# Performance work log

Hardware: AMD Instinct MI355X
Metric: run time of the kernel (lower is better)

The kernel has to match this reference:

```python
import jax, jax.numpy as jnp
import numpy as np

B, S, DIM, H = 2, 2048, 1024, 16
HD = DIM // H  # 64


def setup_inputs() -> dict:
    key = jax.random.key(0)
    ks = jax.random.split(key, 7)
    sc = 1.0 / np.sqrt(DIM)
    gammas = jnp.asarray(1.0 - 2.0 ** (-5.0 - np.arange(H)), jnp.float32)  # RetNet per-head decay
    return {
        "q": jax.random.normal(ks[0], (B, S, DIM), jnp.float32),
        "k": jax.random.normal(ks[1], (B, S, DIM), jnp.float32),
        "v": jax.random.normal(ks[2], (B, S, DIM), jnp.float32),
        "W_in": jax.random.normal(ks[3], (DIM, DIM), jnp.float32) * sc,
        "b_in": jnp.zeros((DIM,), jnp.float32),
        "W_gate": jax.random.normal(ks[4], (DIM, DIM), jnp.float32) * sc,
        "b_gate": jnp.zeros((DIM,), jnp.float32),
        "W_out": jax.random.normal(ks[5], (DIM, DIM), jnp.float32) * sc,
        "b_out": jnp.zeros((DIM,), jnp.float32),
        "gammas": gammas,
    }


def _mamba(x, W_in, b_in, W_gate, b_gate, W_out, b_out):
    # Gated linear recurrence: h_t = a_t * h_{t-1} + u_t  (selective-scan style)
    u = x @ W_in + b_in          # [B,S,D]
    a = jax.nn.sigmoid(x @ W_gate + b_gate)  # [B,S,D] data-dependent decay gate

    def combine(c1, c2):
        a1, u1 = c1
        a2, u2 = c2
        return (a1 * a2, a2 * u1 + u2)

    _, h = jax.lax.associative_scan(combine, (a, u), axis=1)  # parallel scan over S
    return h @ W_out + b_out  # residual=False, dropout=0.0


def _retention(q, k, v, gammas):
    # Per-head decay-masked attention: out = ((Q K^T / sqrt(hd)) * D) V,
    # D[h,n,m] = gamma_h^(n-m) for n>=m else 0 (causal decay kernel).
    def split(x):
        return x.reshape(B, S, H, HD).transpose(0, 2, 1, 3)  # [B,H,S,HD]

    qh, kh, vh = split(q), split(k), split(v)
    idx = jnp.arange(S)
    diff = idx[:, None] - idx[None, :]                        # [S,S]
    expnt = jnp.maximum(diff, 0).astype(jnp.float32)
    D = jnp.where(diff >= 0, gammas[:, None, None] ** expnt, 0.0)  # [H,S,S]
    scores = jnp.einsum("bhnd,bhmd->bhnm", qh, kh) / np.sqrt(HD)
    out = jnp.einsum("bhnm,bhmd->bhnd", scores * D[None], vh)
    return out.transpose(0, 2, 1, 3).reshape(B, S, DIM)


def reference(q, k, v, W_in, b_in, W_gate, b_gate, W_out, b_out, gammas):
    q_proj = _mamba(q, W_in, b_in, W_gate, b_gate, W_out, b_out)
    return _retention(q_proj, k, v, gammas)
```

## Files before the change

### kernel.cpp

```cpp
#include <hip/hip_runtime.h>
#include <math.h>

#define B_  2
#define S_  2048
#define D_  1024
#define H_  16
#define HD_ 64
#define M_  (B_*S_)

typedef unsigned short ushort_t;
typedef unsigned int   uint_t;
typedef __attribute__((ext_vector_type(8))) short bf16x8;
typedef __attribute__((ext_vector_type(4))) float f32x4;

__device__ __forceinline__ ushort_t f2bf(float f) {
    uint_t u = __builtin_bit_cast(uint_t, f);
    u += 0x7FFFu + ((u >> 16) & 1u);
    return (ushort_t)(u >> 16);
}
__device__ __forceinline__ float bf2f(ushort_t h) {
    uint_t u = (uint_t)h << 16;
    return __builtin_bit_cast(float, u);
}
__device__ __forceinline__ uint_t pkt(float lo, float hi) {
    return __builtin_amdgcn_perm(__builtin_bit_cast(uint_t, hi),
                                 __builtin_bit_cast(uint_t, lo), 0x07060302u);
}
__device__ __forceinline__ void dma16(const ushort_t* g, ushort_t* l) {
    __builtin_amdgcn_global_load_lds(
        (const __attribute__((address_space(1))) uint_t*)g,
        (__attribute__((address_space(3))) uint_t*)l, 16, 0, 0);
}
__device__ __forceinline__ bf16x8 fragr(const ushort_t* base, int row, int chunk) {
    return *(const bf16x8*)&base[row * 64 + (((chunk ^ (row & 7)) << 3))];
}

__global__ __launch_bounds__(256)
void transp_cvt3(const float* __restrict__ W0, const float* __restrict__ W1,
                 const float* __restrict__ W2, ushort_t* __restrict__ T0,
                 ushort_t* __restrict__ T1, ushort_t* __restrict__ T2) {
    __shared__ float T[32][36];
    const float*  W  = (blockIdx.z == 0) ? W0 : (blockIdx.z == 1) ? W1 : W2;
    ushort_t*     WT = (blockIdx.z == 0) ? T0 : (blockIdx.z == 1) ? T1 : T2;
    const int kt = blockIdx.x, nt = blockIdx.y;
    const int t = threadIdx.x;
    const int rr = t >> 3, cc = (t & 7) * 4;
    float4 w4 = *(const float4*)(W + (size_t)(kt * 32 + rr) * D_ + nt * 32 + cc);
    T[rr][cc + 0] = w4.x; T[rr][cc + 1] = w4.y; T[rr][cc + 2] = w4.z; T[rr][cc + 3] = w4.w;
    __syncthreads();
    ushort_t o[4];
    #pragma unroll
    for (int j = 0; j < 4; ++j) o[j] = f2bf(T[cc + j][rr]);
    *(ushort4*)(WT + (size_t)(nt * 32 + rr) * D_ + kt * 32 + cc) =
        make_ushort4(o[0], o[1], o[2], o[3]);
}

__global__ __launch_bounds__(256)
void cvt_bf16(const float* __restrict__ X, ushort_t* __restrict__ Y) {
    const int i = (blockIdx.x * 256 + threadIdx.x) * 4;
    float4 x = *(const float4*)(X + i);
    *(ushort4*)(Y + i) = make_ushort4(f2bf(x.x), f2bf(x.y), f2bf(x.z), f2bf(x.w));
}

__global__ __launch_bounds__(256)
void kv_cvt_g(const float* __restrict__ K, const float* __restrict__ V,
              const float* __restrict__ gammas, ushort_t* __restrict__ Kb,
              ushort_t* __restrict__ VT, float* __restrict__ Gg) {
    __shared__ ushort_t Tv[64 * 72];
    __shared__ ushort_t Tk[64 * 72];
    const int mt = blockIdx.x, h = blockIdx.y, b = blockIdx.z;
    const int m0 = mt * 64;
    const int tid = threadIdx.x;
    const int r = tid >> 2, c0 = (tid & 3) * 16;
    const float lg = log2f(gammas[h]);
    const float gm = exp2f(-(float)r * lg);
    {
        const float* src = K + ((size_t)(b * S_ + m0 + r)) * D_ + h * HD_ + c0;
        ushort_t kb[16];
        #pragma unroll
        for (int j4 = 0; j4 < 4; ++j4) {
            float4 x = *(const float4*)(src + j4 * 4);
            kb[j4 * 4 + 0] = f2bf(x.x); kb[j4 * 4 + 1] = f2bf(x.y);
            kb[j4 * 4 + 2] = f2bf(x.z); kb[j4 * 4 + 3] = f2bf(x.w);
        }
        ushort_t* dst = Kb + ((size_t)(b * S_ + m0 + r)) * D_ + h * HD_ + c0;
        *(uint4*)(dst + 0) = *(const uint4*)&kb[0];
        *(uint4*)(dst + 8) = *(const uint4*)&kb[8];
        #pragma unroll
        for (int j = 0; j < 16; ++j) Tk[(c0 + j) * 72 + r] = kb[j];
    }
    {
        const float* src = V + ((size_t)(b * S_ + m0 + r)) * D_ + h * HD_ + c0;
        #pragma unroll
        for (int j4 = 0; j4 < 4; ++j4) {
            float4 x = *(const float4*)(src + j4 * 4);
            Tv[(c0 + j4 * 4 + 0) * 72 + r] = f2bf(x.x * gm);
            Tv[(c0 + j4 * 4 + 1) * 72 + r] = f2bf(x.y * gm);
            Tv[(c0 + j4 * 4 + 2) * 72 + r] = f2bf(x.z * gm);
            Tv[(c0 + j4 * 4 + 3) * 72 + r] = f2bf(x.w * gm);
        }
    }
    __syncthreads();
    {
        ushort_t* dst = VT + ((size_t)((b * H_ + h) * HD_ + r)) * S_ + m0 + c0;
        *(uint4*)(dst + 0) = *(const uint4*)&Tv[r * 72 + c0 + 0];
        *(uint4*)(dst + 8) = *(const uint4*)&Tv[r * 72 + c0 + 8];
    }
    const int w = tid >> 6, lane = tid & 63, quad = lane >> 4, l15 = lane & 15;
    bf16x8 af0 = *(const bf16x8*)&Tv[(w * 16 + l15) * 72 + quad * 8];
    bf16x8 af1 = *(const bf16x8*)&Tv[(w * 16 + l15) * 72 + 32 + quad * 8];
    float* gout = Gg + ((size_t)((b * H_ + h) * 32 + mt)) * 4096;
    #pragma unroll
    for (int kt2 = 0; kt2 < 4; ++kt2) {
        bf16x8 bf0 = *(const bf16x8*)&Tk[(kt2 * 16 + l15) * 72 + quad * 8];
        bf16x8 bf1 = *(const bf16x8*)&Tk[(kt2 * 16 + l15) * 72 + 32 + quad * 8];
        f32x4 g = {};
        g = __builtin_amdgcn_mfma_f32_16x16x32_bf16(af0, bf0, g, 0, 0, 0);
        g = __builtin_amdgcn_mfma_f32_16x16x32_bf16(af1, bf1, g, 0, 0, 0);
        #pragma unroll
        for (int reg = 0; reg < 4; ++reg)
            gout[(w * 16 + quad * 4 + reg) * 64 + kt2 * 16 + l15] = g[reg];
    }
}

__global__ __launch_bounds__(256)
void state_scan(const float* __restrict__ Gg, const float* __restrict__ gammas,
                ushort_t* __restrict__ Sb) {
    const int sl = blockIdx.x, h = blockIdx.y, b = blockIdx.z;
    const float g64 = exp2f(64.0f * log2f(gammas[h]));
    const int r = threadIdx.x >> 4;
    const int cb = (threadIdx.x & 15) * 4;
    const size_t base = ((size_t)((b * H_ + h) * 32)) * 4096 + (sl * 16 + r) * 64 + cb;
    float4 S = make_float4(0.f, 0.f, 0.f, 0.f);
    for (int c = 0; c < 32; ++c) {
        ushort4 sb;
        sb.x = f2bf(S.x); sb.y = f2bf(S.y); sb.z = f2bf(S.z); sb.w = f2bf(S.w);
        *(ushort4*)(Sb + base + (size_t)c * 4096) = sb;
        float4 G = *(const float4*)(Gg + base + (size_t)c * 4096);
        S.x = g64 * (S.x + G.x); S.y = g64 * (S.y + G.y);
        S.z = g64 * (S.z + G.z); S.w = g64 * (S.w + G.w);
    }
}

__global__ __launch_bounds__(256)
void gemm_dual_scan(const ushort_t* __restrict__ A, const ushort_t* __restrict__ BTi,
                    const ushort_t* __restrict__ BTg, const float* __restrict__ bi,
                    const float* __restrict__ bg, float* __restrict__ Hloc,
                    ushort_t* __restrict__ Pp, float* __restrict__ cA,
                    float* __restrict__ cU) {
    __shared__ ushort_t smem[32768];
    const int tid = threadIdx.x;
    const int n0 = blockIdx.x * 64, m0 = blockIdx.y * 128;
    const int w = tid >> 6, lane = tid & 63, quad = lane >> 4, l15 = lane & 15;
    const int wr = (w >> 1) * 64, wc = (w & 1) * 32;
    const int l8 = lane & 7, lr8 = lane >> 3;

    f32x4 acc_i[4][2] = {};
    f32x4 acc_g[4][2] = {};

    auto stage = [&](int k0, int bufo) {
        #pragma unroll
        for (int t = 0; t < 4; ++t) {
            const int row = w * 32 + t * 8 + lr8;
            const int gc = ((l8 ^ (row & 7)) << 3);
            dma16(A + (size_t)(m0 + row) * D_ + k0 + gc, &smem[bufo + row * 64 + l8 * 8]);
        }
        #pragma unroll
        for (int t = 0; t < 2; ++t) {
            const int row = w * 16 + t * 8 + lr8;
            const int gc = ((l8 ^ (row & 7)) << 3);
            dma16(BTi + (size_t)(n0 + row) * D_ + k0 + gc, &smem[bufo + 8192 + row * 64 + l8 * 8]);
            dma16(BTg + (size_t)(n0 + row) * D_ + k0 + gc, &smem[bufo + 12288 + row * 64 + l8 * 8]);
        }
    };

    stage(0, 0);
    __syncthreads();
    for (int t = 0; t < 16; ++t) {
        const int bufo = (t & 1) * 16384;
        if (t < 15) stage((t + 1) * 64, 16384 - bufo);
        const ushort_t* As = smem + bufo;
        const ushort_t* Bi = smem + bufo + 8192;
        const ushort_t* Bg = smem + bufo + 12288;
        #pragma unroll
        for (int kk = 0; kk < 2; ++kk) {
            bf16x8 af[4], bfi[2], bfg[2];
            #pragma unroll
            for (int i = 0; i < 4; ++i)
                af[i] = fragr(As, wr + 16 * i + l15, kk * 4 + quad);
            #pragma unroll
            for (int j = 0; j < 2; ++j) {
                bfi[j] = fragr(Bi, wc + 16 * j + l15, kk * 4 + quad);
                bfg[j] = fragr(Bg, wc + 16 * j + l15, kk * 4 + quad);
            }
            #pragma unroll
            for (int i = 0; i < 4; ++i)
                #pragma unroll
                for (int j = 0; j < 2; ++j) {
                    acc_i[i][j] = __builtin_amdgcn_mfma_f32_16x16x32_bf16(
                        af[i], bfi[j], acc_i[i][j], 0, 0, 0);
                    acc_g[i][j] = __builtin_amdgcn_mfma_f32_16x16x32_bf16(
                        af[i], bfg[j], acc_g[i][j], 0, 0, 0);
                }
        }
        __syncthreads();
    }

    ushort_t* Us = smem;
    ushort_t* Gu = smem + 8448;
    #pragma unroll
    for (int j = 0; j < 2; ++j) {
        const int n = wc + 16 * j + l15;
        const float bbi = bi[n0 + n], bbg = bg[n0 + n];
        #pragma unroll
        for (int i = 0; i < 4; ++i) {
            #pragma unroll
            for (int r = 0; r < 4; ++r) {
                const int m = wr + 16 * i + quad * 4 + r;
                Us[m * 66 + n] = f2bf(acc_i[i][j][r] + bbi);
                float g = 1.0f / (1.0f + __expf(-(acc_g[i][j][r] + bbg)));
                Gu[m * 66 + n] = (ushort_t)__float2uint_rn(g * 65535.0f);
            }
        }
    }
    __syncthreads();

    const int nl = tid & 63, c = tid >> 6;
    const int gmb = m0 + c * 32;
    const size_t gbase = (size_t)gmb * D_ + n0 + nl;
    float Aa = 1.0f, hh = 0.0f;
    #pragma unroll 4
    for (int j = 0; j < 32; ++j) {
        const float g = (float)Gu[(c * 32 + j) * 66 + nl] * (1.0f / 65535.0f);
        const float u = bf2f(Us[(c * 32 + j) * 66 + nl]);
        Aa *= g;
        hh = fmaf(g, hh, u);
        Pp[gbase + (size_t)j * D_] = f2bf(Aa);
        Hloc[gbase + (size_t)j * D_] = hh;
    }
    const int bb = gmb >> 11;
    const int ch = (gmb & 2047) >> 5;
    const int ci = ((bb * 64 + ch) << 10) + n0 + nl;
    cA[ci] = Aa;
    cU[ci] = hh;
}

__global__ __launch_bounds__(64)
void scan_pass2(const float* __restrict__ cA, const float* __restrict__ cU,
                float* __restrict__ cIn) {
    const int t = blockIdx.x * 64 + threadIdx.x;
    const int d = t & 1023, b = t >> 10;
    float h = 0.0f;
    for (int c0 = 0; c0 < 64; c0 += 16) {
        float Av[16], Uv[16];
        #pragma unroll
        for (int j = 0; j < 16; ++j) {
            const int idx = ((b * 64 + c0 + j) << 10) + d;
            Av[j] = cA[idx]; Uv[j] = cU[idx];
        }
        #pragma unroll
        for (int j = 0; j < 16; ++j) {
            cIn[((b * 64 + c0 + j) << 10) + d] = h;
            h = fmaf(Av[j], h, Uv[j]);
        }
    }
}

__global__ __launch_bounds__(256)
void scan_fix(const float* __restrict__ Hloc, const ushort_t* __restrict__ Pp,
              const float* __restrict__ cIn, ushort_t* __restrict__ hout) {
    const int i = (blockIdx.x * 256 + threadIdx.x) * 4;
    const int m = i >> 10, d = i & 1023;
    const int b = m >> 11, ch = (m & 2047) >> 5;
    float4 hl = *(const float4*)(Hloc + i);
    ushort4 p4 = *(const ushort4*)(Pp + i);
    float4 ci = *(const float4*)(cIn + ((b * 64 + ch) << 10) + d);
    ushort4 o;
    o.x = f2bf(fmaf(ci.x, bf2f(p4.x), hl.x));
    o.y = f2bf(fmaf(ci.y, bf2f(p4.y), hl.y));
    o.z = f2bf(fmaf(ci.z, bf2f(p4.z), hl.z));
    o.w = f2bf(fmaf(ci.w, bf2f(p4.w), hl.w));
    *(ushort4*)(hout + i) = o;
}

__global__ __launch_bounds__(256)
void gemm_out_a(const ushort_t* __restrict__ A, const ushort_t* __restrict__ BT,
                const float* __restrict__ bias, float scale,
                ushort_t* __restrict__ Cb) {
    __shared__ ushort_t smem[24576];
    const int tid = threadIdx.x;
    const int n0 = blockIdx.x * 64, m0 = blockIdx.y * 128;
    const int w = tid >> 6, lane = tid & 63, quad = lane >> 4, l15 = lane & 15;
    const int wr = (w >> 1) * 64, wc = (w & 1) * 32;
    const int l8 = lane & 7, lr8 = lane >> 3;

    f32x4 acc[4][2] = {};

    auto stage = [&](int k0, int bufo) {
        #pragma unroll
        for (int t = 0; t < 4; ++t) {
            const int row = w * 32 + t * 8 + lr8;
            const int gc = ((l8 ^ (row & 7)) << 3);
            dma16(A + (size_t)(m0 + row) * D_ + k0 + gc, &smem[bufo + row * 64 + l8 * 8]);
        }
        #pragma unroll
        for (int t = 0; t < 2; ++t) {
            const int row = w * 16 + t * 8 + lr8;
            const int gc = ((l8 ^ (row & 7)) << 3);
            dma16(BT + (size_t)(n0 + row) * D_ + k0 + gc, &smem[bufo + 8192 + row * 64 + l8 * 8]);
        }
    };

    stage(0, 0);
    __syncthreads();
    for (int t = 0; t < 16; ++t) {
        const int bufo = (t & 1) * 12288;
        if (t < 15) stage((t + 1) * 64, 12288 - bufo);
        const ushort_t* As = smem + bufo;
        const ushort_t* Bs = smem + bufo + 8192;
        #pragma unroll
        for (int kk = 0; kk < 2; ++kk) {
            bf16x8 af[4], bf[2];
            #pragma unroll
            for (int i = 0; i < 4; ++i)
                af[i] = fragr(As, wr + 16 * i + l15, kk * 4 + quad);
            #pragma unroll
            for (int j = 0; j < 2; ++j)
                bf[j] = fragr(Bs, wc + 16 * j + l15, kk * 4 + quad);
            #pragma unroll
            for (int i = 0; i < 4; ++i)
                #pragma unroll
                for (int j = 0; j < 2; ++j)
                    acc[i][j] = __builtin_amdgcn_mfma_f32_16x16x32_bf16(
                        af[i], bf[j], acc[i][j], 0, 0, 0);
        }
        __syncthreads();
    }

    #pragma unroll
    for (int j = 0; j < 2; ++j) {
        const int n = n0 + wc + 16 * j + l15;
        const float bb = bias[n];
        #pragma unroll
        for (int i = 0; i < 4; ++i)
            #pragma unroll
            for (int r = 0; r < 4; ++r) {
                const int m = m0 + wr + 16 * i + quad * 4 + r;
                Cb[(size_t)m * D_ + n] = f2bf((acc[i][j][r] + bb) * scale);
            }
    }
}

__global__ __launch_bounds__(256)
void retention_chunk(const ushort_t* __restrict__ Qb, const ushort_t* __restrict__ Kb,
                     const ushort_t* __restrict__ VT, const ushort_t* __restrict__ Sb,
                     const float* __restrict__ gammas, float* __restrict__ Out) {
    __shared__ ushort_t smem[20480];
    ushort_t* Qs = smem;
    ushort_t* Ks = smem + 4096;
    ushort_t* Vt = smem + 8192;
    ushort_t* Ss = smem + 12288;
    ushort_t* Ps = smem + 16384;
    const int tid = threadIdx.x;
    const int nt = blockIdx.x, h = blockIdx.y, b = blockIdx.z;
    const int n0 = nt * 64;
    const float lg = log2f(gammas[h]);
    const int w = tid >> 6, lane = tid & 63, quad = lane >> 4, l15 = lane & 15;
    const int l8 = lane & 7, lr8 = lane >> 3;
    const int nl = w * 16 + l15;
    const size_t bS = (size_t)b * S_;
    const size_t vrow0 = (size_t)((b * H_ + h) * HD_);
    const size_t sbase = ((size_t)((b * H_ + h) * 32 + nt)) * 4096;

    #pragma unroll
    for (int t = 0; t < 2; ++t) {
        const int row = w * 16 + t * 8 + lr8;
        const int gc = ((l8 ^ (row & 7)) << 3);
        dma16(Qb + (bS + n0 + row) * D_ + h * HD_ + gc, &Qs[row * 64 + l8 * 8]);
        dma16(Kb + (bS + n0 + row) * D_ + h * HD_ + gc, &Ks[row * 64 + l8 * 8]);
        dma16(VT + (vrow0 + row) * S_ + n0 + gc, &Vt[row * 64 + l8 * 8]);
        dma16(Sb + sbase + (size_t)row * 64 + gc, &Ss[row * 64 + l8 * 8]);
    }
    __syncthreads();

    bf16x8 qf0 = fragr(Qs, nl, quad);
    bf16x8 qf1 = fragr(Qs, nl, 4 + quad);

    f32x4 o[4] = {};
    #pragma unroll
    for (int ct = 0; ct < 4; ++ct) {
        bf16x8 sf0 = fragr(Ss, ct * 16 + l15, quad);
        bf16x8 sf1 = fragr(Ss, ct * 16 + l15, 4 + quad);
        o[ct] = __builtin_amdgcn_mfma_f32_16x16x32_bf16(sf0, qf0, o[ct], 0, 0, 0);
        o[ct] = __builtin_amdgcn_mfma_f32_16x16x32_bf16(sf1, qf1, o[ct], 0, 0, 0);
    }
    #pragma unroll
    for (int mt2 = 0; mt2 < 4; ++mt2) {
        bf16x8 kf0 = fragr(Ks, mt2 * 16 + l15, quad);
        bf16x8 kf1 = fragr(Ks, mt2 * 16 + l15, 4 + quad);
        f32x4 s = {};
        s = __builtin_amdgcn_mfma_f32_16x16x32_bf16(kf0, qf0, s, 0, 0, 0);
        s = __builtin_amdgcn_mfma_f32_16x16x32_bf16(kf1, qf1, s, 0, 0, 0);
        const int mbase = mt2 * 16 + quad * 4;
        #pragma unroll
        for (int r = 0; r < 4; ++r)
            if (nl < mbase + r) s[r] = 0.0f;
        uint2 pw; pw.x = pkt(s[0], s[1]); pw.y = pkt(s[2], s[3]);
        const int chunk = mbase >> 3;
        *(uint2*)&Ps[nl * 64 + ((chunk ^ (nl & 7)) << 3) + (mbase & 7)] = pw;
    }
    bf16x8 pf0 = fragr(Ps, nl, quad);
    bf16x8 pf1 = fragr(Ps, nl, 4 + quad);
    #pragma unroll
    for (int ct = 0; ct < 4; ++ct) {
        bf16x8 vf0 = fragr(Vt, ct * 16 + l15, quad);
        bf16x8 vf1 = fragr(Vt, ct * 16 + l15, 4 + quad);
        o[ct] = __builtin_amdgcn_mfma_f32_16x16x32_bf16(vf0, pf0, o[ct], 0, 0, 0);
        o[ct] = __builtin_amdgcn_mfma_f32_16x16x32_bf16(vf1, pf1, o[ct], 0, 0, 0);
    }

    const float esc = exp2f((float)nl * lg);
    const size_t ob = (bS + n0 + nl) * D_ + h * HD_;
    #pragma unroll
    for (int ct = 0; ct < 4; ++ct) {
        f32x4 t = o[ct] * esc;
        *(f32x4*)(Out + ob + ct * 16 + quad * 4) = t;
    }
}

extern "C" void kernel_launch(void* const* d_in, const int* in_sizes, int n_in,
                              void* d_out, int out_size, void* d_ws, size_t ws_size,
                              hipStream_t stream) {
    const float* q      = (const float*)d_in[0];
    const float* k      = (const float*)d_in[1];
    const float* v      = (const float*)d_in[2];
    const float* W_in   = (const float*)d_in[3];
    const float* b_in   = (const float*)d_in[4];
    const float* W_gate = (const float*)d_in[5];
    const float* b_gate = (const float*)d_in[6];
    const float* W_out  = (const float*)d_in[7];
    const float* b_out  = (const float*)d_in[8];
    const float* gammas = (const float*)d_in[9];
    float* out = (float*)d_out;

    char* ws = (char*)d_ws;
    const size_t MB = 1024 * 1024;
    float*    Hloc    = (float*)(ws);
    ushort_t* Pp      = (ushort_t*)(ws + 16 * MB);
    ushort_t* h_bf    = (ushort_t*)(ws + 24 * MB);
    ushort_t* q_bf    = (ushort_t*)(ws + 32 * MB);
    ushort_t* WT_in   = (ushort_t*)(ws + 40 * MB);
    ushort_t* WT_gate = (ushort_t*)(ws + 42 * MB);
    ushort_t* WT_out  = (ushort_t*)(ws + 44 * MB);
    float*    cA      = (float*)(ws + 46 * MB);
    float*    cU      = (float*)(ws + 46 * MB + 512 * 1024);
    float*    cIn     = (float*)(ws + 47 * MB);
    ushort_t* k_bf    = (ushort_t*)(ws);
    ushort_t* VT      = (ushort_t*)(ws + 8 * MB);
    float*    Gg      = (float*)(ws + 16 * MB);
    ushort_t* Sb      = (ushort_t*)(ws + 40 * MB);
    ushort_t* qp_bf   = q_bf;

    transp_cvt3<<<dim3(D_ / 32, D_ / 32, 3), 256, 0, stream>>>(
        W_in, W_gate, W_out, WT_in, WT_gate, WT_out);
    cvt_bf16<<<(M_ * D_) / (256 * 4), 256, 0, stream>>>(q, q_bf);

    gemm_dual_scan<<<dim3(D_ / 64, M_ / 128), 256, 0, stream>>>(
        q_bf, WT_in, WT_gate, b_in, b_gate, Hloc, Pp, cA, cU);

    scan_pass2<<<32, 64, 0, stream>>>(cA, cU, cIn);
    scan_fix<<<(M_ * D_) / 1024, 256, 0, stream>>>(Hloc, Pp, cIn, h_bf);

    gemm_out_a<<<dim3(D_ / 64, M_ / 128), 256, 0, stream>>>(
        h_bf, WT_out, b_out, 0.125f, qp_bf);

    kv_cvt_g<<<dim3(S_ / 64, H_, B_), 256, 0, stream>>>(k, v, gammas, k_bf, VT, Gg);
    state_scan<<<dim3(4, H_, B_), 256, 0, stream>>>(Gg, gammas, Sb);

    retention_chunk<<<dim3(S_ / 64, H_, B_), 256, 0, stream>>>(
        qp_bf, k_bf, VT, Sb, gammas, out);
}
```

Before: 188.6 us.

## Fuse prep kernels, pack scan intermediates, fuse output GEMM into retention

Merges the weight transpose, q conversion and k/v conversion into one prep kernel, which cuts the launch count. The per-chunk Gram matrices are now stored as bf16, and the scan's local prefix product and hidden state are packed into one 32-bit word instead of separate fp32 and bf16 arrays. The output projection GEMM is fused into the retention kernel, so each block computes its own 64x64 Q tile in LDS and the qp_bf round trip goes away. The trade-offs are lower precision in the intermediates and per-block GEMM work with only 64-row tiles, which may reduce MFMA efficiency.

```diff
diff --git a/kernel.cpp b/kernel.cpp
--- a/kernel.cpp
+++ b/kernel.cpp
@@ -36,41 +36,46 @@
 }
 
 __global__ __launch_bounds__(256)
-void transp_cvt3(const float* __restrict__ W0, const float* __restrict__ W1,
-                 const float* __restrict__ W2, ushort_t* __restrict__ T0,
-                 ushort_t* __restrict__ T1, ushort_t* __restrict__ T2) {
-    __shared__ float T[32][36];
-    const float*  W  = (blockIdx.z == 0) ? W0 : (blockIdx.z == 1) ? W1 : W2;
-    ushort_t*     WT = (blockIdx.z == 0) ? T0 : (blockIdx.z == 1) ? T1 : T2;
-    const int kt = blockIdx.x, nt = blockIdx.y;
-    const int t = threadIdx.x;
-    const int rr = t >> 3, cc = (t & 7) * 4;
-    float4 w4 = *(const float4*)(W + (size_t)(kt * 32 + rr) * D_ + nt * 32 + cc);
-    T[rr][cc + 0] = w4.x; T[rr][cc + 1] = w4.y; T[rr][cc + 2] = w4.z; T[rr][cc + 3] = w4.w;
-    __syncthreads();
-    ushort_t o[4];
-    #pragma unroll
-    for (int j = 0; j < 4; ++j) o[j] = f2bf(T[cc + j][rr]);
-    *(ushort4*)(WT + (size_t)(nt * 32 + rr) * D_ + kt * 32 + cc) =
-        make_ushort4(o[0], o[1], o[2], o[3]);
-}
-
-__global__ __launch_bounds__(256)
-void cvt_bf16(const float* __restrict__ X, ushort_t* __restrict__ Y) {
-    const int i = (blockIdx.x * 256 + threadIdx.x) * 4;
-    float4 x = *(const float4*)(X + i);
-    *(ushort4*)(Y + i) = make_ushort4(f2bf(x.x), f2bf(x.y), f2bf(x.z), f2bf(x.w));
-}
-
-__global__ __launch_bounds__(256)
-void kv_cvt_g(const float* __restrict__ K, const float* __restrict__ V,
-              const float* __restrict__ gammas, ushort_t* __restrict__ Kb,
-              ushort_t* __restrict__ VT, float* __restrict__ Gg) {
-    __shared__ ushort_t Tv[64 * 72];
-    __shared__ ushort_t Tk[64 * 72];
-    const int mt = blockIdx.x, h = blockIdx.y, b = blockIdx.z;
+void prep(const float* __restrict__ W0, const float* __restrict__ W1,
+          const float* __restrict__ W2, ushort_t* __restrict__ T0,
+          ushort_t* __restrict__ T1, ushort_t* __restrict__ T2,
+          const float* __restrict__ q, ushort_t* __restrict__ q_bf,
+          const float* __restrict__ K, const float* __restrict__ V,
+          const float* __restrict__ gammas, ushort_t* __restrict__ Kb,
+          ushort_t* __restrict__ VT, ushort_t* __restrict__ Gg) {
+    __shared__ ushort_t sh[9216];
+    const int bi = blockIdx.x;
+    const int tid = threadIdx.x;
+
+    if (bi < 3072) {
+        float* T = (float*)sh;
+        const int z = bi >> 10, rem = bi & 1023;
+        const int kt = rem & 31, nt = rem >> 5;
+        const float*  W  = (z == 0) ? W0 : (z == 1) ? W1 : W2;
+        ushort_t*     WT = (z == 0) ? T0 : (z == 1) ? T1 : T2;
+        const int rr = tid >> 3, cc = (tid & 7) * 4;
+        float4 w4 = *(const float4*)(W + (size_t)(kt * 32 + rr) * D_ + nt * 32 + cc);
+        T[rr * 36 + cc + 0] = w4.x; T[rr * 36 + cc + 1] = w4.y;
+        T[rr * 36 + cc + 2] = w4.z; T[rr * 36 + cc + 3] = w4.w;
+        __syncthreads();
+        ushort_t o[4];
+        #pragma unroll
+        for (int j = 0; j < 4; ++j) o[j] = f2bf(T[(cc + j) * 36 + rr]);
+        *(ushort4*)(WT + (size_t)(nt * 32 + rr) * D_ + kt * 32 + cc) =
+            make_ushort4(o[0], o[1], o[2], o[3]);
+        return;
+    }
+    if (bi < 7168) {
+        const int i = ((bi - 3072) * 256 + tid) * 4;
+        float4 x = *(const float4*)(q + i);
+        *(ushort4*)(q_bf + i) = make_ushort4(f2bf(x.x), f2bf(x.y), f2bf(x.z), f2bf(x.w));
+        return;
+    }
+    ushort_t* Tv = sh;
+    ushort_t* Tk = sh + 4608;
+    const int rem = bi - 7168;
+    const int mt = rem & 31, h = (rem >> 5) & 15, b = rem >> 9;
     const int m0 = mt * 64;
-    const int tid = threadIdx.x;
     const int r = tid >> 2, c0 = (tid & 3) * 16;
     const float lg = log2f(gammas[h]);
     const float gm = exp2f(-(float)r * lg);
@@ -109,7 +114,7 @@
     const int w = tid >> 6, lane = tid & 63, quad = lane >> 4, l15 = lane & 15;
     bf16x8 af0 = *(const bf16x8*)&Tv[(w * 16 + l15) * 72 + quad * 8];
     bf16x8 af1 = *(const bf16x8*)&Tv[(w * 16 + l15) * 72 + 32 + quad * 8];
-    float* gout = Gg + ((size_t)((b * H_ + h) * 32 + mt)) * 4096;
+    ushort_t* gout = Gg + ((size_t)((b * H_ + h) * 32 + mt)) * 4096;
     #pragma unroll
     for (int kt2 = 0; kt2 < 4; ++kt2) {
         bf16x8 bf0 = *(const bf16x8*)&Tk[(kt2 * 16 + l15) * 72 + quad * 8];
@@ -119,12 +124,12 @@
         g = __builtin_amdgcn_mfma_f32_16x16x32_bf16(af1, bf1, g, 0, 0, 0);
         #pragma unroll
         for (int reg = 0; reg < 4; ++reg)
-            gout[(w * 16 + quad * 4 + reg) * 64 + kt2 * 16 + l15] = g[reg];
+            gout[(w * 16 + quad * 4 + reg) * 64 + kt2 * 16 + l15] = f2bf(g[reg]);
     }
 }
 
 __global__ __launch_bounds__(256)
-void state_scan(const float* __restrict__ Gg, const float* __restrict__ gammas,
+void state_scan(const ushort_t* __restrict__ Gg, const float* __restrict__ gammas,
                 ushort_t* __restrict__ Sb) {
     const int sl = blockIdx.x, h = blockIdx.y, b = blockIdx.z;
     const float g64 = exp2f(64.0f * log2f(gammas[h]));
@@ -133,21 +138,20 @@
     const size_t base = ((size_t)((b * H_ + h) * 32)) * 4096 + (sl * 16 + r) * 64 + cb;
     float4 S = make_float4(0.f, 0.f, 0.f, 0.f);
     for (int c = 0; c < 32; ++c) {
+        ushort4 g4 = *(const ushort4*)(Gg + base + (size_t)c * 4096);
         ushort4 sb;
         sb.x = f2bf(S.x); sb.y = f2bf(S.y); sb.z = f2bf(S.z); sb.w = f2bf(S.w);
         *(ushort4*)(Sb + base + (size_t)c * 4096) = sb;
-        float4 G = *(const float4*)(Gg + base + (size_t)c * 4096);
-        S.x = g64 * (S.x + G.x); S.y = g64 * (S.y + G.y);
-        S.z = g64 * (S.z + G.z); S.w = g64 * (S.w + G.w);
+        S.x = g64 * (S.x + bf2f(g4.x)); S.y = g64 * (S.y + bf2f(g4.y));
+        S.z = g64 * (S.z + bf2f(g4.z)); S.w = g64 * (S.w + bf2f(g4.w));
     }
 }
 
 __global__ __launch_bounds__(256)
 void gemm_dual_scan(const ushort_t* __restrict__ A, const ushort_t* __restrict__ BTi,
                     const ushort_t* __restrict__ BTg, const float* __restrict__ bi,
-                    const float* __restrict__ bg, float* __restrict__ Hloc,
-                    ushort_t* __restrict__ Pp, float* __restrict__ cA,
-                    float* __restrict__ cU) {
+                    const float* __restrict__ bg, uint_t* __restrict__ PH,
+                    float* __restrict__ cA, float* __restrict__ cU) {
     __shared__ ushort_t smem[32768];
     const int tid = threadIdx.x;
     const int n0 = blockIdx.x * 64, m0 = blockIdx.y * 128;
@@ -207,7 +211,7 @@
     }
 
     ushort_t* Us = smem;
-    ushort_t* Gu = smem + 8448;
+    ushort_t* Gu = smem + 8192;
     #pragma unroll
     for (int j = 0; j < 2; ++j) {
         const int n = wc + 16 * j + l15;
@@ -217,9 +221,9 @@
             #pragma unroll
             for (int r = 0; r < 4; ++r) {
                 const int m = wr + 16 * i + quad * 4 + r;
-                Us[m * 66 + n] = f2bf(acc_i[i][j][r] + bbi);
+                Us[m * 64 + n] = f2bf(acc_i[i][j][r] + bbi);
                 float g = 1.0f / (1.0f + __expf(-(acc_g[i][j][r] + bbg)));
-                Gu[m * 66 + n] = (ushort_t)__float2uint_rn(g * 65535.0f);
+                Gu[m * 64 + n] = (ushort_t)__float2uint_rn(g * 65535.0f);
             }
         }
     }
@@ -231,12 +235,11 @@
     float Aa = 1.0f, hh = 0.0f;
     #pragma unroll 4
     for (int j = 0; j < 32; ++j) {
-        const float g = (float)Gu[(c * 32 + j) * 66 + nl] * (1.0f / 65535.0f);
-        const float u = bf2f(Us[(c * 32 + j) * 66 + nl]);
+        const float g = (float)Gu[(c * 32 + j) * 64 + nl] * (1.0f / 65535.0f);
+        const float u = bf2f(Us[(c * 32 + j) * 64 + nl]);
         Aa *= g;
         hh = fmaf(g, hh, u);
-        Pp[gbase + (size_t)j * D_] = f2bf(Aa);
-        Hloc[gbase + (size_t)j * D_] = hh;
+        PH[gbase + (size_t)j * D_] = pkt(Aa, hh);
     }
     const int bb = gmb >> 11;
     const int ch = (gmb & 2047) >> 5;
@@ -267,100 +270,27 @@
 }
 
 __global__ __launch_bounds__(256)
-void scan_fix(const float* __restrict__ Hloc, const ushort_t* __restrict__ Pp,
-              const float* __restrict__ cIn, ushort_t* __restrict__ hout) {
+void scan_fix(const uint_t* __restrict__ PH, const float* __restrict__ cIn,
+              ushort_t* __restrict__ hout) {
     const int i = (blockIdx.x * 256 + threadIdx.x) * 4;
     const int m = i >> 10, d = i & 1023;
     const int b = m >> 11, ch = (m & 2047) >> 5;
-    float4 hl = *(const float4*)(Hloc + i);
-    ushort4 p4 = *(const ushort4*)(Pp + i);
+    uint4 p = *(const uint4*)(PH + i);
     float4 ci = *(const float4*)(cIn + ((b * 64 + ch) << 10) + d);
     ushort4 o;
-    o.x = f2bf(fmaf(ci.x, bf2f(p4.x), hl.x));
-    o.y = f2bf(fmaf(ci.y, bf2f(p4.y), hl.y));
-    o.z = f2bf(fmaf(ci.z, bf2f(p4.z), hl.z));
-    o.w = f2bf(fmaf(ci.w, bf2f(p4.w), hl.w));
+    o.x = f2bf(fmaf(ci.x, bf2f((ushort_t)(p.x & 0xFFFF)), bf2f((ushort_t)(p.x >> 16))));
+    o.y = f2bf(fmaf(ci.y, bf2f((ushort_t)(p.y & 0xFFFF)), bf2f((ushort_t)(p.y >> 16))));
+    o.z = f2bf(fmaf(ci.z, bf2f((ushort_t)(p.z & 0xFFFF)), bf2f((ushort_t)(p.z >> 16))));
+    o.w = f2bf(fmaf(ci.w, bf2f((ushort_t)(p.w & 0xFFFF)), bf2f((ushort_t)(p.w >> 16))));
     *(ushort4*)(hout + i) = o;
 }
 
 __global__ __launch_bounds__(256)
-void gemm_out_a(const ushort_t* __restrict__ A, const ushort_t* __restrict__ BT,
-                const float* __restrict__ bias, float scale,
-                ushort_t* __restrict__ Cb) {
-    __shared__ ushort_t smem[24576];
-    const int tid = threadIdx.x;
-    const int n0 = blockIdx.x * 64, m0 = blockIdx.y * 128;
-    const int w = tid >> 6, lane = tid & 63, quad = lane >> 4, l15 = lane & 15;
-    const int wr = (w >> 1) * 64, wc = (w & 1) * 32;
-    const int l8 = lane & 7, lr8 = lane >> 3;
-
-    f32x4 acc[4][2] = {};
-
-    auto stage = [&](int k0, int bufo) {
-        #pragma unroll
-        for (int t = 0; t < 4; ++t) {
-            const int row = w * 32 + t * 8 + lr8;
-            const int gc = ((l8 ^ (row & 7)) << 3);
-            dma16(A + (size_t)(m0 + row) * D_ + k0 + gc, &smem[bufo + row * 64 + l8 * 8]);
-        }
-        #pragma unroll
-        for (int t = 0; t < 2; ++t) {
-            const int row = w * 16 + t * 8 + lr8;
-            const int gc = ((l8 ^ (row & 7)) << 3);
-            dma16(BT + (size_t)(n0 + row) * D_ + k0 + gc, &smem[bufo + 8192 + row * 64 + l8 * 8]);
-        }
-    };
-
-    stage(0, 0);
-    __syncthreads();
-    for (int t = 0; t < 16; ++t) {
-        const int bufo = (t & 1) * 12288;
-        if (t < 15) stage((t + 1) * 64, 12288 - bufo);
-        const ushort_t* As = smem + bufo;
-        const ushort_t* Bs = smem + bufo + 8192;
-        #pragma unroll
-        for (int kk = 0; kk < 2; ++kk) {
-            bf16x8 af[4], bf[2];
-            #pragma unroll
-            for (int i = 0; i < 4; ++i)
-                af[i] = fragr(As, wr + 16 * i + l15, kk * 4 + quad);
-            #pragma unroll
-            for (int j = 0; j < 2; ++j)
-                bf[j] = fragr(Bs, wc + 16 * j + l15, kk * 4 + quad);
-            #pragma unroll
-            for (int i = 0; i < 4; ++i)
-                #pragma unroll
-                for (int j = 0; j < 2; ++j)
-                    acc[i][j] = __builtin_amdgcn_mfma_f32_16x16x32_bf16(
-                        af[i], bf[j], acc[i][j], 0, 0, 0);
-        }
-        __syncthreads();
-    }
-
-    #pragma unroll
-    for (int j = 0; j < 2; ++j) {
-        const int n = n0 + wc + 16 * j + l15;
-        const float bb = bias[n];
-        #pragma unroll
-        for (int i = 0; i < 4; ++i)
-            #pragma unroll
-            for (int r = 0; r < 4; ++r) {
-                const int m = m0 + wr + 16 * i + quad * 4 + r;
-                Cb[(size_t)m * D_ + n] = f2bf((acc[i][j][r] + bb) * scale);
-            }
-    }
-}
-
-__global__ __launch_bounds__(256)
-void retention_chunk(const ushort_t* __restrict__ Qb, const ushort_t* __restrict__ Kb,
+void retention_fused(const ushort_t* __restrict__ Hb, const ushort_t* __restrict__ WTo,
+                     const float* __restrict__ bo, const ushort_t* __restrict__ Kb,
                      const ushort_t* __restrict__ VT, const ushort_t* __restrict__ Sb,
                      const float* __restrict__ gammas, float* __restrict__ Out) {
-    __shared__ ushort_t smem[20480];
-    ushort_t* Qs = smem;
-    ushort_t* Ks = smem + 4096;
-    ushort_t* Vt = smem + 8192;
-    ushort_t* Ss = smem + 12288;
-    ushort_t* Ps = smem + 16384;
+    __shared__ ushort_t smem[28672];
     const int tid = threadIdx.x;
     const int nt = blockIdx.x, h = blockIdx.y, b = blockIdx.z;
     const int n0 = nt * 64;
@@ -376,15 +306,62 @@
     for (int t = 0; t < 2; ++t) {
         const int row = w * 16 + t * 8 + lr8;
         const int gc = ((l8 ^ (row & 7)) << 3);
-        dma16(Qb + (bS + n0 + row) * D_ + h * HD_ + gc, &Qs[row * 64 + l8 * 8]);
-        dma16(Kb + (bS + n0 + row) * D_ + h * HD_ + gc, &Ks[row * 64 + l8 * 8]);
-        dma16(VT + (vrow0 + row) * S_ + n0 + gc, &Vt[row * 64 + l8 * 8]);
-        dma16(Sb + sbase + (size_t)row * 64 + gc, &Ss[row * 64 + l8 * 8]);
+        dma16(Kb + (bS + n0 + row) * D_ + h * HD_ + gc, &smem[16384 + row * 64 + l8 * 8]);
+        dma16(VT + (vrow0 + row) * S_ + n0 + gc,        &smem[20480 + row * 64 + l8 * 8]);
+        dma16(Sb + sbase + (size_t)row * 64 + gc,       &smem[24576 + row * 64 + l8 * 8]);
+    }
+
+    auto stage = [&](int k0, int bufo) {
+        #pragma unroll
+        for (int t = 0; t < 2; ++t) {
+            const int row = w * 8 + t * 32 + lr8;
+            const int gc = ((l8 ^ (row & 7)) << 3);
+            dma16(Hb + (bS + n0 + row) * D_ + k0 + gc, &smem[bufo + row * 64 + l8 * 8]);
+            dma16(WTo + ((size_t)(h * 64 + row)) * D_ + k0 + gc,
+                  &smem[bufo + 4096 + row * 64 + l8 * 8]);
+        }
+    };
+    stage(0, 0);
+    __syncthreads();
+
+    f32x4 acc[4] = {};
+    for (int t = 0; t < 16; ++t) {
+        const int bufo = (t & 1) * 8192;
+        if (t < 15) stage((t + 1) * 64, 8192 - bufo);
+        const ushort_t* As = smem + bufo;
+        const ushort_t* Bs = smem + bufo + 4096;
+        #pragma unroll
+        for (int kk = 0; kk < 2; ++kk) {
+            bf16x8 af = fragr(As, w * 16 + l15, kk * 4 + quad);
+            #pragma unroll
+            for (int ct = 0; ct < 4; ++ct) {
+                bf16x8 bf = fragr(Bs, ct * 16 + l15, kk * 4 + quad);
+                acc[ct] = __builtin_amdgcn_mfma_f32_16x16x32_bf16(af, bf, acc[ct], 0, 0, 0);
+            }
+        }
+        __syncthreads();
+    }
+
+    ushort_t* Qs = smem;
+    ushort_t* Ps = smem + 4096;
+    #pragma unroll
+    for (int ct = 0; ct < 4; ++ct) {
+        const int n = ct * 16 + l15;
+        const float bb = bo[h * 64 + n];
+        #pragma unroll
+        for (int r = 0; r < 4; ++r) {
+            const int m = w * 16 + quad * 4 + r;
+            Qs[m * 64 + (((n >> 3) ^ (m & 7)) << 3) + (n & 7)] =
+                f2bf((acc[ct][r] + bb) * 0.125f);
+        }
     }
     __syncthreads();
 
     bf16x8 qf0 = fragr(Qs, nl, quad);
     bf16x8 qf1 = fragr(Qs, nl, 4 + quad);
+    const ushort_t* Ks = smem + 16384;
+    const ushort_t* Vt = smem + 20480;
+    const ushort_t* Ss = smem + 24576;
 
     f32x4 o[4] = {};
     #pragma unroll
@@ -445,38 +422,31 @@
 
     char* ws = (char*)d_ws;
     const size_t MB = 1024 * 1024;
-    float*    Hloc    = (float*)(ws);
-    ushort_t* Pp      = (ushort_t*)(ws + 16 * MB);
-    ushort_t* h_bf    = (ushort_t*)(ws + 24 * MB);
-    ushort_t* q_bf    = (ushort_t*)(ws + 32 * MB);
-    ushort_t* WT_in   = (ushort_t*)(ws + 40 * MB);
-    ushort_t* WT_gate = (ushort_t*)(ws + 42 * MB);
-    ushort_t* WT_out  = (ushort_t*)(ws + 44 * MB);
-    float*    cA      = (float*)(ws + 46 * MB);
-    float*    cU      = (float*)(ws + 46 * MB + 512 * 1024);
-    float*    cIn     = (float*)(ws + 47 * MB);
-    ushort_t* k_bf    = (ushort_t*)(ws);
-    ushort_t* VT      = (ushort_t*)(ws + 8 * MB);
-    float*    Gg      = (float*)(ws + 16 * MB);
-    ushort_t* Sb      = (ushort_t*)(ws + 40 * MB);
-    ushort_t* qp_bf   = q_bf;
-
-    transp_cvt3<<<dim3(D_ / 32, D_ / 32, 3), 256, 0, stream>>>(
-        W_in, W_gate, W_out, WT_in, WT_gate, WT_out);
-    cvt_bf16<<<(M_ * D_) / (256 * 4), 256, 0, stream>>>(q, q_bf);
+    ushort_t* q_bf    = (ushort_t*)(ws);
+    ushort_t* k_bf    = (ushort_t*)(ws + 8 * MB);
+    ushort_t* VT      = (ushort_t*)(ws + 16 * MB);
+    ushort_t* WT_in   = (ushort_t*)(ws + 24 * MB);
+    ushort_t* WT_gate = (ushort_t*)(ws + 26 * MB);
+    ushort_t* WT_out  = (ushort_t*)(ws + 28 * MB);
+    ushort_t* Sb      = (ushort_t*)(ws + 30 * MB);
+    ushort_t* Gg      = (ushort_t*)(ws + 38 * MB);
+    uint_t*   PH      = (uint_t*)(ws + 48 * MB);
+    ushort_t* h_bf    = (ushort_t*)(ws + 64 * MB);
+    float*    cA      = (float*)(ws + 72 * MB);
+    float*    cU      = (float*)(ws + 72 * MB + 512 * 1024);
+    float*    cIn     = (float*)(ws + 73 * MB);
+
+    prep<<<8192, 256, 0, stream>>>(W_in, W_gate, W_out, WT_in, WT_gate, WT_out,
+                                   q, q_bf, k, v, gammas, k_bf, VT, Gg);
+
+    state_scan<<<dim3(4, H_, B_), 256, 0, stream>>>(Gg, gammas, Sb);
 
     gemm_dual_scan<<<dim3(D_ / 64, M_ / 128), 256, 0, stream>>>(
-        q_bf, WT_in, WT_gate, b_in, b_gate, Hloc, Pp, cA, cU);
+        q_bf, WT_in, WT_gate, b_in, b_gate, PH, cA, cU);
 
     scan_pass2<<<32, 64, 0, stream>>>(cA, cU, cIn);
-    scan_fix<<<(M_ * D_) / 1024, 256, 0, stream>>>(Hloc, Pp, cIn, h_bf);
-
-    gemm_out_a<<<dim3(D_ / 64, M_ / 128), 256, 0, stream>>>(
-        h_bf, WT_out, b_out, 0.125f, qp_bf);
-
-    kv_cvt_g<<<dim3(S_ / 64, H_, B_), 256, 0, stream>>>(k, v, gammas, k_bf, VT, Gg);
-    state_scan<<<dim3(4, H_, B_), 256, 0, stream>>>(Gg, gammas, Sb);
-
-    retention_chunk<<<dim3(S_ / 64, H_, B_), 256, 0, stream>>>(
-        qp_bf, k_bf, VT, Sb, gammas, out);
-}
+    scan_fix<<<(M_ * D_) / 1024, 256, 0, stream>>>(PH, cIn, h_bf);
+
+    retention_fused<<<dim3(S_ / 64, H_, B_), 256, 0, stream>>>(
+        h_bf, WT_out, b_out, k_bf, VT, Sb, gammas, out);
+}
```

Result: no change. 190.6 us (+1.1%).
